# Kernel tuning notes

Hardware: AMD Instinct MI355X
Metric: run time of the kernel (lower is better)

The kernel has to match this reference:

```python
import jax, jax.numpy as jnp
import numpy as np
from jax import lax

VOCAB = 5000
BLANK = 0          # vocab.unk_id
SMOOTHING = 0.1    # config.model.label_smoothing
ALPHA = 0.2        # config.model.alpha
NEG = -1e30        # finite stand-in for -inf (stable under logaddexp)


def setup_inputs() -> dict:
    key = jax.random.key(0)
    k1, k2, k3 = jax.random.split(key, 3)
    att_logits = jax.random.normal(k1, (16, 128, VOCAB), dtype=jnp.float32)
    ctc_logits = jax.random.normal(k2, (16, 512, VOCAB), dtype=jnp.float32)
    targets = jax.random.randint(k3, (16, 128), 0, VOCAB)
    return {"att_logits": att_logits, "ctc_logits": ctc_logits, "targets": targets}


def _label_smoothing_loss(logit_bsv, targets_bs):
    # torch: label_smoothed filled with smoothing/(V-1), confidence at target;
    # loss = mean over rows of sum(-label_smoothed * logit).
    B, S, V = logit_bsv.shape
    logit = logit_bsv.reshape(-1, V)                       # (B*S, V)
    tgt = targets_bs.reshape(-1)                           # (B*S,)
    confidence = 1.0 - SMOOTHING
    off = SMOOTHING / (V - 1)
    tgt_logit = jnp.take_along_axis(logit, tgt[:, None], axis=1)[:, 0]
    row_sum = jnp.sum(logit, axis=-1)
    # sum(-ls*logit) = -(confidence*logit[t] + off*(row_sum - logit[t]))
    per_row = -(confidence * tgt_logit + off * (row_sum - tgt_logit))
    return jnp.mean(per_row)


def _ctc_loss(log_probs_btv, targets_bs):
    # torch nn.CTCLoss(blank=BLANK, reduction='mean', zero_infinity=True)
    # input is time-major log-probs (T, B, V); full lengths on both sides.
    lp = jnp.transpose(log_probs_btv, (1, 0, 2))           # (T, B, V)
    T, B, V = lp.shape
    S = targets_bs.shape[1]
    L = 2 * S + 1
    # extended target: blank interleaved
    ext = jnp.full((B, L), BLANK, dtype=targets_bs.dtype).at[:, 1::2].set(targets_bs)
    # emission log-probs per extended symbol: (T, B, L)
    emit = jnp.take_along_axis(lp, jnp.broadcast_to(ext[None], (T, B, L)), axis=2)
    # skip (s-2) transition allowed when ext[s] != blank and ext[s] != ext[s-2]
    ext_m2 = jnp.roll(ext, 2, axis=1)
    allow2 = (ext != BLANK) & (ext != ext_m2)
    allow2 = allow2.at[:, :2].set(False)
    alpha0 = jnp.full((B, L), NEG, dtype=lp.dtype)
    alpha0 = alpha0.at[:, 0].set(emit[0, :, 0]).at[:, 1].set(emit[0, :, 1])

    negpad1 = jnp.full((B, 1), NEG, dtype=lp.dtype)
    negpad2 = jnp.full((B, 2), NEG, dtype=lp.dtype)

    def step(alpha, e_t):
        a1 = jnp.concatenate([negpad1, alpha[:, :-1]], axis=1)
        a2 = jnp.concatenate([negpad2, alpha[:, :-2]], axis=1)
        a2 = jnp.where(allow2, a2, NEG)
        new = jnp.logaddexp(jnp.logaddexp(alpha, a1), a2) + e_t
        return new, None

    alphaT, _ = lax.scan(step, alpha0, emit[1:])
    ll = jnp.logaddexp(alphaT[:, L - 1], alphaT[:, L - 2])
    loss_b = -ll                                           # (B,)
    # zero_infinity: invalid paths (loss ~ 1e30) -> 0
    loss_b = jnp.where(loss_b > 1e20, 0.0, loss_b)
    # reduction='mean': divide by target length, then mean over batch
    return jnp.mean(loss_b / S)


def reference(att_logits, ctc_logits, targets):
    att_loss = _label_smoothing_loss(att_logits, targets)
    ctc_loss = _ctc_loss(ctc_logits, targets)
    return ALPHA * att_loss + (1.0 - ALPHA) * ctc_loss
```

## Files before the change

kernel.cpp:

```cpp
#include <hip/hip_runtime.h>
#include <math.h>

#define VOCAB   5000
#define T_CTC   512
#define S_TGT   128
#define BATCH   16
#define ALPHA_W 0.2f
#define CONF    0.9f
#define OFFV    (0.1f / 4999.0f)
#define CHUNK   64
#define NCHUNK  8
#define CSTR    132
#define ATT_N   (BATCH * S_TGT)
#define WS_OFF  4096
#define GATHER_BLKS (BATCH * (T_CTC / 2))

__global__ __launch_bounds__(256)
void gather_att_kernel(const float* __restrict__ ctc,
                       const float* __restrict__ att,
                       const int*   __restrict__ tgt,
                       float*       __restrict__ ws)
{
    if (blockIdx.x < GATHER_BLKS) {
        const int b     = blockIdx.x >> 8;
        const int tpair = blockIdx.x & 255;
        const int t0    = 2 * tpair;

        __shared__ int tg[S_TGT];
        if (threadIdx.x < S_TGT) tg[threadIdx.x] = tgt[b * S_TGT + threadIdx.x];
        __syncthreads();

        const float* lp   = ctc + (size_t)b * T_CTC * VOCAB;
        float*       cbuf = ws + WS_OFF + ((size_t)b * T_CTC) * CSTR;

        for (int v = threadIdx.x; v < 258; v += 256) {
            const int tt  = (v < 129) ? 0 : 1;
            const int idx = (v < 129) ? v : v - 129;
            const int col = (idx < 128) ? tg[idx] : 0;
            cbuf[(size_t)(t0 + tt) * CSTR + idx] = lp[(size_t)(t0 + tt) * VOCAB + col];
        }
        return;
    }

    const int rr = blockIdx.x - GATHER_BLKS;
    const float* row = att + (size_t)rr * VOCAB;
    const float4* row4 = (const float4*)row;

    float sum = 0.0f;
    for (int i = threadIdx.x; i < VOCAB / 4; i += 256) {
        float4 v = row4[i];
        sum += v.x + v.y + v.z + v.w;
    }
    #pragma unroll
    for (int off = 32; off > 0; off >>= 1)
        sum += __shfl_down(sum, off, 64);

    __shared__ float wsum[4];
    if ((threadIdx.x & 63) == 0) wsum[threadIdx.x >> 6] = sum;
    __syncthreads();
    if (threadIdx.x == 0) {
        const float rs = wsum[0] + wsum[1] + wsum[2] + wsum[3];
        const float tl = row[tgt[rr]];
        ws[rr] = -(CONF * tl + OFFV * (rs - tl));
    }
}

__global__ __launch_bounds__(512)
void ctc_kernel(const int* __restrict__ tgt, float* __restrict__ ws)
{
    __shared__ __align__(16) float ebuf[2][CHUNK][CSTR];

    const int b    = blockIdx.x;
    const int tid  = threadIdx.x;
    const int wave = tid >> 6;
    const int lane = tid & 63;
    const int*   tg   = tgt + b * S_TGT;
    const float* cbuf = ws + WS_OFF + ((size_t)b * T_CTC) * CSTR;

    {
        const float4* src = (const float4*)(cbuf + (size_t)1 * CSTR);
        float4*       dst = (float4*)&ebuf[0][0][0];
        for (int i = tid; i < CHUNK * (CSTR / 4); i += 512) dst[i] = src[i];
    }

    const int k  = lane;
    const int t1 = tg[2 * k];
    const int t3 = tg[2 * k + 1];
    const int tp = (k > 0) ? tg[2 * k - 1] : 0;
    const double g1 = ((k > 0) && (t1 != 0) && (t1 != tp)) ? 1.0 : 0.0;
    const double g3 = ((t3 != 0) && (t3 != t1)) ? 1.0 : 0.0;

    const float e00 = cbuf[128];
    double M  = (double)e00;
    double b0 = (k == 0) ? 1.0 : 0.0;
    double b1 = (k == 0) ? (double)__expf(cbuf[0] - e00) : 0.0;
    double b2 = 0.0, b3 = 0.0, b4 = 0.0;

    __syncthreads();

    for (int c = 0; c < NCHUNK; ++c) {
        const int buf = c & 1;
        if (wave == 0) {
            const int tbase = 1 + c * CHUNK;
            #pragma unroll
            for (int h = 0; h < CHUNK / 16; ++h) {
                double X1[16], X3[16];
                float  Z[16];
                #pragma unroll
                for (int i = 0; i < 16; ++i) {
                    const int st = h * 16 + i;
                    const float2 e13 = *reinterpret_cast<const float2*>(&ebuf[buf][st][2 * k]);
                    const float  e0  = ebuf[buf][st][128];
                    X1[i] = (double)__expf(e13.x - e0);
                    X3[i] = (double)__expf(e13.y - e0);
                    Z[i]  = e0;
                }
                #pragma unroll
                for (int i = 0; i < 16; ++i) {
                    if (tbase + h * 16 + i < T_CTC) {
                        double p3 = __shfl_up(b3, 1, 64);
                        p3 = (k == 0) ? 0.0 : p3;
                        const double n0 = b0 + p3;
                        const double n1 = (b1 + b0 + g1 * p3) * X1[i];
                        const double n2 = b2 + b1;
                        const double n3 = (b3 + b2 + g3 * b1) * X3[i];
                        const double n4 = b4 + b3;
                        b0 = n0; b1 = n1; b2 = n2; b3 = n3; b4 = n4;
                        M += (double)Z[i];
                    }
                }
            }
        } else if (c + 1 < NCHUNK) {
            const int nbuf  = buf ^ 1;
            const int tbase = 1 + (c + 1) * CHUNK;
            const int rows  = min(CHUNK, T_CTC - tbase);
            const float4* src = (const float4*)(cbuf + (size_t)tbase * CSTR);
            float4*       dst = (float4*)&ebuf[nbuf][0][0];
            const int n4v = rows * (CSTR / 4);
            for (int i = tid - 64; i < n4v; i += 448) dst[i] = src[i];
        }
        __syncthreads();
    }

    if (wave == 0 && k == 63) {
        const double bsum = b3 + b4;
        const double ll   = M + log(bsum);
        float loss_b = (float)(-ll);
        if (!(loss_b <= 1e20f)) loss_b = 0.0f;
        ws[ATT_N + b] = loss_b;
    }
}

__global__ __launch_bounds__(256)
void combine_kernel(const float* __restrict__ ws, float* __restrict__ out)
{
    const int tid = threadIdx.x;
    float s_att = 0.0f;
    for (int i = tid; i < ATT_N; i += 256) s_att += ws[i];
    float s_ctc = (tid < BATCH) ? ws[ATT_N + tid] : 0.0f;

    #pragma unroll
    for (int off = 32; off > 0; off >>= 1) {
        s_att += __shfl_down(s_att, off, 64);
        s_ctc += __shfl_down(s_ctc, off, 64);
    }
    __shared__ float wa[4], wc[4];
    if ((tid & 63) == 0) { wa[tid >> 6] = s_att; wc[tid >> 6] = s_ctc; }
    __syncthreads();
    if (tid == 0) {
        const float inv = 1.0f / (float)ATT_N;
        const float a = (wa[0] + wa[1] + wa[2] + wa[3]) * inv;
        const float c = (wc[0] + wc[1] + wc[2] + wc[3]) * inv;
        out[0] = ALPHA_W * a + (1.0f - ALPHA_W) * c;
    }
}

extern "C" void kernel_launch(void* const* d_in, const int* in_sizes, int n_in,
                              void* d_out, int out_size, void* d_ws, size_t ws_size,
                              hipStream_t stream)
{
    const float* att = (const float*)d_in[0];
    const float* ctc = (const float*)d_in[1];
    const int*   tgt = (const int*)d_in[2];
    float* out = (float*)d_out;
    float* ws  = (float*)d_ws;

    gather_att_kernel<<<GATHER_BLKS + ATT_N, 256, 0, stream>>>(ctc, att, tgt, ws);
    ctc_kernel<<<BATCH, 512, 0, stream>>>(tgt, ws);
    combine_kernel<<<1, 256, 0, stream>>>(ws, out);
}
```

Measured before the change: 285.6 us.

## Move CTC emission exp and log-scale sum into producer waves

The producer waves now turn the staged emission values into normalized probabilities (exp of e - e_blank) while copying them into shared memory. They also reduce the per-chunk blank log-prob sum into a small shared array. This takes the exp and the M accumulation out of the serial recurrence wave, which now only loads float2 pairs and runs fully unrolled 8-step groups without per-step bounds checks. The gather kernel also drops its shared staging of targets. The cost is more work per element in the producer waves, and scalar strided global loads in place of float4 copies.

```diff
diff --git a/kernel.cpp b/kernel.cpp
--- a/kernel.cpp
+++ b/kernel.cpp
@@ -11,9 +11,13 @@
 #define CHUNK   64
 #define NCHUNK  8
 #define CSTR    132
-#define ATT_N   (BATCH * S_TGT)
-#define WS_OFF  4096
-#define GATHER_BLKS (BATCH * (T_CTC / 2))
+
+#define WS_ATT   0
+#define WS_CTC   2048
+#define WS_CBUF  4096
+
+#define GATHER_BLKS 4096
+#define ATT_N       2048
 
 __global__ __launch_bounds__(256)
 void gather_att_kernel(const float* __restrict__ ctc,
@@ -25,17 +29,13 @@
         const int b     = blockIdx.x >> 8;
         const int tpair = blockIdx.x & 255;
         const int t0    = 2 * tpair;
-
-        __shared__ int tg[S_TGT];
-        if (threadIdx.x < S_TGT) tg[threadIdx.x] = tgt[b * S_TGT + threadIdx.x];
-        __syncthreads();
-
         const float* lp   = ctc + (size_t)b * T_CTC * VOCAB;
-        float*       cbuf = ws + WS_OFF + ((size_t)b * T_CTC) * CSTR;
+        const int*   tg   = tgt + b * S_TGT;
+        float*       cbuf = ws + WS_CBUF + (size_t)b * T_CTC * CSTR;
 
         for (int v = threadIdx.x; v < 258; v += 256) {
-            const int tt  = (v < 129) ? 0 : 1;
-            const int idx = (v < 129) ? v : v - 129;
+            const int tt  = (v >= 129) ? 1 : 0;
+            const int idx = v - 129 * tt;
             const int col = (idx < 128) ? tg[idx] : 0;
             cbuf[(size_t)(t0 + tt) * CSTR + idx] = lp[(size_t)(t0 + tt) * VOCAB + col];
         }
@@ -61,26 +61,51 @@
     if (threadIdx.x == 0) {
         const float rs = wsum[0] + wsum[1] + wsum[2] + wsum[3];
         const float tl = row[tgt[rr]];
-        ws[rr] = -(CONF * tl + OFFV * (rs - tl));
-    }
-}
+        ws[WS_ATT + rr] = -(CONF * tl + OFFV * (rs - tl));
+    }
+}
+
+#define STEP(j) {                                                   \
+    double E1 = (double)Ej[j].x, E3 = (double)Ej[j].y;              \
+    double p3 = __shfl_up(b3, 1, 64); p3 = (k == 0) ? 0.0 : p3;     \
+    double n0 = b0 + p3;                                            \
+    double n1 = (b1 + b0 + g1 * p3) * E1;                           \
+    double n2 = b2 + b1;                                            \
+    double n3 = (b3 + b2 + g3 * b1) * E3;                           \
+    double n4 = b4 + b3;                                            \
+    b0 = n0; b1 = n1; b2 = n2; b3 = n3; b4 = n4; }
+
+#define GROUP(N, R0) {                                              \
+    float2 Ej[N];                                                   \
+    _Pragma("unroll")                                               \
+    for (int j = 0; j < (N); ++j)                                   \
+        Ej[j] = *(const float2*)&ebuf[bs][(R0) + j][2 * k];         \
+    _Pragma("unroll")                                               \
+    for (int j = 0; j < (N); ++j) STEP(j) }
 
 __global__ __launch_bounds__(512)
 void ctc_kernel(const int* __restrict__ tgt, float* __restrict__ ws)
 {
-    __shared__ __align__(16) float ebuf[2][CHUNK][CSTR];
+    __shared__ __align__(16) float ebuf[2][CHUNK][128];
+    __shared__ double e0sumS[NCHUNK];
 
     const int b    = blockIdx.x;
     const int tid  = threadIdx.x;
     const int wave = tid >> 6;
     const int lane = tid & 63;
     const int*   tg   = tgt + b * S_TGT;
-    const float* cbuf = ws + WS_OFF + ((size_t)b * T_CTC) * CSTR;
-
-    {
-        const float4* src = (const float4*)(cbuf + (size_t)1 * CSTR);
-        float4*       dst = (float4*)&ebuf[0][0][0];
-        for (int i = tid; i < CHUNK * (CSTR / 4); i += 512) dst[i] = src[i];
+    const float* cbuf = ws + WS_CBUF + (size_t)b * T_CTC * CSTR;
+
+    for (int idx = tid; idx < CHUNK * 128; idx += 512) {
+        const int row = idx >> 7, s = idx & 127;
+        const float* cr = cbuf + (size_t)(1 + row) * CSTR;
+        ebuf[0][row][s] = __expf(cr[s] - cr[128]);
+    }
+    if (wave == 1) {
+        double v = (double)cbuf[(size_t)(1 + lane) * CSTR + 128];
+        #pragma unroll
+        for (int off = 32; off > 0; off >>= 1) v += __shfl_down(v, off, 64);
+        if (lane == 0) e0sumS[0] = v;
     }
 
     const int k  = lane;
@@ -91,63 +116,48 @@
     const double g3 = ((t3 != 0) && (t3 != t1)) ? 1.0 : 0.0;
 
     const float e00 = cbuf[128];
-    double M  = (double)e00;
     double b0 = (k == 0) ? 1.0 : 0.0;
     double b1 = (k == 0) ? (double)__expf(cbuf[0] - e00) : 0.0;
     double b2 = 0.0, b3 = 0.0, b4 = 0.0;
-
     __syncthreads();
 
     for (int c = 0; c < NCHUNK; ++c) {
-        const int buf = c & 1;
+        const int bs = c & 1;
         if (wave == 0) {
-            const int tbase = 1 + c * CHUNK;
-            #pragma unroll
-            for (int h = 0; h < CHUNK / 16; ++h) {
-                double X1[16], X3[16];
-                float  Z[16];
-                #pragma unroll
-                for (int i = 0; i < 16; ++i) {
-                    const int st = h * 16 + i;
-                    const float2 e13 = *reinterpret_cast<const float2*>(&ebuf[buf][st][2 * k]);
-                    const float  e0  = ebuf[buf][st][128];
-                    X1[i] = (double)__expf(e13.x - e0);
-                    X3[i] = (double)__expf(e13.y - e0);
-                    Z[i]  = e0;
-                }
-                #pragma unroll
-                for (int i = 0; i < 16; ++i) {
-                    if (tbase + h * 16 + i < T_CTC) {
-                        double p3 = __shfl_up(b3, 1, 64);
-                        p3 = (k == 0) ? 0.0 : p3;
-                        const double n0 = b0 + p3;
-                        const double n1 = (b1 + b0 + g1 * p3) * X1[i];
-                        const double n2 = b2 + b1;
-                        const double n3 = (b3 + b2 + g3 * b1) * X3[i];
-                        const double n4 = b4 + b3;
-                        b0 = n0; b1 = n1; b2 = n2; b3 = n3; b4 = n4;
-                        M += (double)Z[i];
-                    }
-                }
+            if (c < NCHUNK - 1) {
+                GROUP(8, 0)  GROUP(8, 8)  GROUP(8, 16) GROUP(8, 24)
+                GROUP(8, 32) GROUP(8, 40) GROUP(8, 48) GROUP(8, 56)
+            } else {
+                GROUP(8, 0)  GROUP(8, 8)  GROUP(8, 16) GROUP(8, 24)
+                GROUP(8, 32) GROUP(8, 40) GROUP(8, 48) GROUP(7, 56)
             }
         } else if (c + 1 < NCHUNK) {
-            const int nbuf  = buf ^ 1;
+            const int nb    = bs ^ 1;
             const int tbase = 1 + (c + 1) * CHUNK;
             const int rows  = min(CHUNK, T_CTC - tbase);
-            const float4* src = (const float4*)(cbuf + (size_t)tbase * CSTR);
-            float4*       dst = (float4*)&ebuf[nbuf][0][0];
-            const int n4v = rows * (CSTR / 4);
-            for (int i = tid - 64; i < n4v; i += 448) dst[i] = src[i];
+            for (int idx = tid - 64; idx < rows * 128; idx += 448) {
+                const int row = idx >> 7, s = idx & 127;
+                const float* cr = cbuf + (size_t)(tbase + row) * CSTR;
+                ebuf[nb][row][s] = __expf(cr[s] - cr[128]);
+            }
+            if (wave == 1) {
+                double v = (lane < rows) ? (double)cbuf[(size_t)(tbase + lane) * CSTR + 128] : 0.0;
+                #pragma unroll
+                for (int off = 32; off > 0; off >>= 1) v += __shfl_down(v, off, 64);
+                if (lane == 0) e0sumS[c + 1] = v;
+            }
         }
         __syncthreads();
     }
 
     if (wave == 0 && k == 63) {
-        const double bsum = b3 + b4;
-        const double ll   = M + log(bsum);
+        double M = (double)e00;
+        #pragma unroll
+        for (int c = 0; c < NCHUNK; ++c) M += e0sumS[c];
+        const double ll = M + log(b3 + b4);
         float loss_b = (float)(-ll);
         if (!(loss_b <= 1e20f)) loss_b = 0.0f;
-        ws[ATT_N + b] = loss_b;
+        ws[WS_CTC + b] = loss_b;
     }
 }
 
@@ -156,8 +166,8 @@
 {
     const int tid = threadIdx.x;
     float s_att = 0.0f;
-    for (int i = tid; i < ATT_N; i += 256) s_att += ws[i];
-    float s_ctc = (tid < BATCH) ? ws[ATT_N + tid] : 0.0f;
+    for (int i = tid; i < ATT_N; i += 256) s_att += ws[WS_ATT + i];
+    float s_ctc = (tid < BATCH) ? ws[WS_CTC + tid] : 0.0f;
 
     #pragma unroll
     for (int off = 32; off > 0; off >>= 1) {
```

New measurement: 291.9 us. 2.2% more time.
